# Kernel optimization log

Measured on AMD Instinct MI355X. Metric: run time of the kernel, lower is better.

## Reference

```python
import jax, jax.numpy as jnp
import numpy as np
from jax import lax

K = 12          # filterbank order (units per group)
G = 2           # number of groups / filterbanks
T_SAMP = 1.0    # samp_interval
B, S = 2048, 2048


def setup_inputs() -> dict:
    key = jax.random.key(0)
    k1, k2 = jax.random.split(key)
    x = jax.random.normal(k1, (B, S, G), dtype=jnp.float32)
    # relax in (0.2, 0.8) so sqrt(relax) and sqrt(1-relax) are well-behaved
    relax = 0.2 + 0.6 * jax.random.uniform(k2, (G,), dtype=jnp.float32)
    return {"x": x, "relax": relax}


def reference(x, relax):
    """Laguerre FilterbankCell unrolled over time with lax.scan.

    x:     [B, S, G] input sequence (one channel per filterbank group)
    relax: [G]       per-group relaxation parameter in (0,1)
    returns [B, S, G, K] filterbank outputs per timestep.
    """
    sa = jnp.sqrt(relax)            # sqrt(relax_i),    [G]
    sb = jnp.sqrt(1.0 - relax)      # sqrt(1-relax_i),  [G]

    def step(prev, xt):
        # prev: [B, G, K] previous filterbank state; xt: [B, G]
        y0 = sa[None, :] * prev[:, :, 0] + T_SAMP * sb[None, :] * xt  # [B, G]
        ys = [y0]
        for j in range(1, K):  # K is small and fixed -> unrolled lag chain
            yj = sa[None, :] * prev[:, :, j] + sa[None, :] * ys[-1] - prev[:, :, j - 1]
            ys.append(yj)
        y = jnp.stack(ys, axis=2)  # [B, G, K]
        return y, y

    init = jnp.zeros((x.shape[0], G, K), dtype=x.dtype)
    xs = jnp.moveaxis(x, 1, 0)                 # [S, B, G]
    _, outs = lax.scan(step, init, xs)         # [S, B, G, K]
    return jnp.moveaxis(outs, 0, 1)            # [B, S, G, K]
```

## Files before the change

kernel.cpp:

```cpp
#include <hip/hip_runtime.h>


#define KF 12
#define GF 2
#define BF 2048
#define SF 2048
#define CHUNKS 32
#define LCH 64
#define BG (BF * GF)

__global__ void setup_mpow(const float* __restrict__ relax, float* __restrict__ Mp) {
    const int g = blockIdx.x;
    const int t = threadIdx.x;
    __shared__ float A[KF][KF];
    const float rx = relax[g];
    const float sa = sqrtf(rx);

    if (t < KF * KF) {
        const int j = t / KF, m = t % KF;
        float v = 0.0f;
        if (m == j) {
            v = sa;
        } else if (m < j) {
            float p = 1.0f;
            for (int i = 0; i < j - m - 1; ++i) p *= sa;
            v = -(1.0f - rx) * p;
        }
        A[j][m] = v;
    }
    __syncthreads();

    for (int it = 0; it < 6; ++it) {
        float s = 0.0f;
        if (t < KF * KF) {
            const int j = t / KF, m = t % KF;
            #pragma unroll
            for (int i = 0; i < KF; ++i) s += A[j][i] * A[i][m];
        }
        __syncthreads();
        if (t < KF * KF) A[t / KF][t % KF] = s;
        __syncthreads();
    }

    if (t < KF * KF) Mp[g * KF * KF + t] = A[t / KF][t % KF];
}

__device__ __forceinline__ void fb_step(float* y, float xt, float sa, float tsb) {
    float pm1 = y[0];
    y[0] = sa * y[0] + tsb * xt;
    #pragma unroll
    for (int j = 1; j < KF; ++j) {
        const float tmp = y[j];
        y[j] = sa * tmp + sa * y[j - 1] - pm1;
        pm1 = tmp;
    }
}

__global__ void pass1_chunk_states(const float* __restrict__ x,
                                   const float* __restrict__ relax,
                                   float* __restrict__ F) {
    const int tid = blockIdx.x * blockDim.x + threadIdx.x;
    const int g = tid & 1;
    const int b = (tid >> 1) & (BF - 1);
    const int c = tid >> 12;

    const float rx = relax[g];
    const float sa = sqrtf(rx);
    const float tsb = sqrtf(1.0f - rx);

    float y[KF];
    #pragma unroll
    for (int k = 0; k < KF; ++k) y[k] = 0.0f;

    const float* xp = x + ((size_t)b * SF + (size_t)c * LCH) * GF + g;
    for (int t = 0; t < LCH; ++t) {
        fb_step(y, xp[(size_t)t * GF], sa, tsb);
    }

    float4* Fp = (float4*)(F + (((size_t)c * BF + b) * GF + g) * KF);
    Fp[0] = make_float4(y[0], y[1], y[2],  y[3]);
    Fp[1] = make_float4(y[4], y[5], y[6],  y[7]);
    Fp[2] = make_float4(y[8], y[9], y[10], y[11]);
}

__global__ void pass2_combine(float* __restrict__ F, const float* __restrict__ Mp) {
    const int tid = blockIdx.x * blockDim.x + threadIdx.x;
    const int sub = tid & 15;
    const int bg  = tid >> 4;
    const int g   = bg & 1;
    const int lane = threadIdx.x & 63;
    const int grpbase = lane & ~15;

    const int k = (sub < KF) ? sub : 0;
    float Mrow[KF];
    const float* mr = Mp + ((size_t)g * KF + k) * KF;
    #pragma unroll
    for (int m = 0; m < KF; ++m) Mrow[m] = mr[m];

    float r = 0.0f;
    for (int c = 1; c < CHUNKS; ++c) {
        float* slot = F + ((size_t)(c - 1) * BG + bg) * KF + k;
        const float f = *slot;
        float acc = f;
        #pragma unroll
        for (int m = 0; m < KF; ++m) {
            acc += Mrow[m] * __shfl(r, grpbase + m, 64);
        }
        if (sub < KF) *slot = acc;
        r = acc;
    }
}

__global__ void pass3_outputs(const float* __restrict__ x,
                              const float* __restrict__ relax,
                              const float* __restrict__ F,
                              float* __restrict__ out) {
    const int tid = blockIdx.x * blockDim.x + threadIdx.x;
    const int g = tid & 1;
    const int b = (tid >> 1) & (BF - 1);
    const int c = tid >> 12;

    const float rx = relax[g];
    const float sa = sqrtf(rx);
    const float tsb = sqrtf(1.0f - rx);

    float y[KF];
    if (c == 0) {
        #pragma unroll
        for (int k = 0; k < KF; ++k) y[k] = 0.0f;
    } else {
        const float4* Fp = (const float4*)(F + ((size_t)(c - 1) * BG + (b * GF + g)) * KF);
        const float4 a0 = Fp[0], a1 = Fp[1], a2 = Fp[2];
        y[0] = a0.x; y[1] = a0.y; y[2]  = a0.z; y[3]  = a0.w;
        y[4] = a1.x; y[5] = a1.y; y[6]  = a1.z; y[7]  = a1.w;
        y[8] = a2.x; y[9] = a2.y; y[10] = a2.z; y[11] = a2.w;
    }

    const float* xp = x + ((size_t)b * SF + (size_t)c * LCH) * GF + g;
    float* op = out + (((size_t)b * SF + (size_t)c * LCH) * GF + g) * KF;

    for (int t = 0; t < LCH; ++t) {
        fb_step(y, xp[(size_t)t * GF], sa, tsb);
        float4* o4 = (float4*)(op + (size_t)t * (GF * KF));
        o4[0] = make_float4(y[0], y[1], y[2],  y[3]);
        o4[1] = make_float4(y[4], y[5], y[6],  y[7]);
        o4[2] = make_float4(y[8], y[9], y[10], y[11]);
    }
}

extern "C" void kernel_launch(void* const* d_in, const int* in_sizes, int n_in,
                              void* d_out, int out_size, void* d_ws, size_t ws_size,
                              hipStream_t stream) {
    const float* x     = (const float*)d_in[0];
    const float* relax = (const float*)d_in[1];
    float* out = (float*)d_out;

    float* Mp = (float*)d_ws;
    float* F  = (float*)((char*)d_ws + 4096);

    setup_mpow<<<GF, 192, 0, stream>>>(relax, Mp);

    const int threads13 = BG * CHUNKS;
    pass1_chunk_states<<<threads13 / 256, 256, 0, stream>>>(x, relax, F);

    pass2_combine<<<(BG * 16) / 256, 256, 0, stream>>>(F, Mp);

    pass3_outputs<<<threads13 / 256, 256, 0, stream>>>(x, relax, F, out);
}
```

Before: 573.6 us.

## Process both groups per thread and raise chunk count for more parallelism

Each thread in pass1 and pass3 now runs the filter for both groups together, reading x as float4 and writing the 24 outputs of a timestep together. The chunk index becomes the fastest-varying thread index, and the chunk count rises to 128 (or 64 if workspace is small), with shorter chunks and a matching matrix power. This aims at more instruction-level parallelism and better load vectorization. The cost is more register pressure, a longer serial pass2 combine chain, and more scattered output stores across adjacent threads.

```diff
diff --git a/kernel.cpp b/kernel.cpp
--- a/kernel.cpp
+++ b/kernel.cpp
@@ -5,11 +5,27 @@
 #define GF 2
 #define BF 2048
 #define SF 2048
-#define CHUNKS 32
-#define LCH 64
 #define BG (BF * GF)
 
+__device__ __forceinline__ void fb_step2(float* __restrict__ y0, float* __restrict__ y1,
+                                         float x0, float x1,
+                                         float sa0, float tsb0, float sa1, float tsb1) {
+    float pm0 = y0[0], pm1 = y1[0];
+    y0[0] = fmaf(sa0, y0[0], tsb0 * x0);
+    y1[0] = fmaf(sa1, y1[0], tsb1 * x1);
+    #pragma unroll
+    for (int j = 1; j < KF; ++j) {
+        const float t0 = y0[j], t1 = y1[j];
+        y0[j] = fmaf(sa0, t0, fmaf(sa0, y0[j - 1], -pm0));
+        y1[j] = fmaf(sa1, t1, fmaf(sa1, y1[j - 1], -pm1));
+        pm0 = t0; pm1 = t1;
+    }
+}
+
+template <int NC>
 __global__ void setup_mpow(const float* __restrict__ relax, float* __restrict__ Mp) {
+    constexpr int LCH = SF / NC;
+    constexpr int LOG2L = (LCH == 16) ? 4 : ((LCH == 32) ? 5 : 6);
     const int g = blockIdx.x;
     const int t = threadIdx.x;
     __shared__ float A[KF][KF];
@@ -30,7 +46,7 @@
     }
     __syncthreads();
 
-    for (int it = 0; it < 6; ++it) {
+    for (int it = 0; it < LOG2L; ++it) {
         float s = 0.0f;
         if (t < KF * KF) {
             const int j = t / KF, m = t % KF;
@@ -45,44 +61,41 @@
     if (t < KF * KF) Mp[g * KF * KF + t] = A[t / KF][t % KF];
 }
 
-__device__ __forceinline__ void fb_step(float* y, float xt, float sa, float tsb) {
-    float pm1 = y[0];
-    y[0] = sa * y[0] + tsb * xt;
+template <int NC>
+__global__ __launch_bounds__(256, 4) void pass1_chunk_states(
+        const float* __restrict__ x, const float* __restrict__ relax,
+        float* __restrict__ F) {
+    constexpr int LCH = SF / NC;
+    const int tid = blockIdx.x * 256 + threadIdx.x;
+    const int c = tid & (NC - 1);
+    const int b = tid / NC;
+
+    const float r0 = relax[0], r1 = relax[1];
+    const float sa0 = sqrtf(r0), tsb0 = sqrtf(1.0f - r0);
+    const float sa1 = sqrtf(r1), tsb1 = sqrtf(1.0f - r1);
+
+    float y0[KF], y1[KF];
     #pragma unroll
-    for (int j = 1; j < KF; ++j) {
-        const float tmp = y[j];
-        y[j] = sa * tmp + sa * y[j - 1] - pm1;
-        pm1 = tmp;
-    }
-}
-
-__global__ void pass1_chunk_states(const float* __restrict__ x,
-                                   const float* __restrict__ relax,
-                                   float* __restrict__ F) {
-    const int tid = blockIdx.x * blockDim.x + threadIdx.x;
-    const int g = tid & 1;
-    const int b = (tid >> 1) & (BF - 1);
-    const int c = tid >> 12;
-
-    const float rx = relax[g];
-    const float sa = sqrtf(rx);
-    const float tsb = sqrtf(1.0f - rx);
-
-    float y[KF];
-    #pragma unroll
-    for (int k = 0; k < KF; ++k) y[k] = 0.0f;
-
-    const float* xp = x + ((size_t)b * SF + (size_t)c * LCH) * GF + g;
-    for (int t = 0; t < LCH; ++t) {
-        fb_step(y, xp[(size_t)t * GF], sa, tsb);
-    }
-
-    float4* Fp = (float4*)(F + (((size_t)c * BF + b) * GF + g) * KF);
-    Fp[0] = make_float4(y[0], y[1], y[2],  y[3]);
-    Fp[1] = make_float4(y[4], y[5], y[6],  y[7]);
-    Fp[2] = make_float4(y[8], y[9], y[10], y[11]);
-}
-
+    for (int k = 0; k < KF; ++k) { y0[k] = 0.0f; y1[k] = 0.0f; }
+
+    const float4* xp = (const float4*)(x + ((size_t)b * SF + (size_t)c * LCH) * GF);
+    #pragma unroll 2
+    for (int t2 = 0; t2 < LCH / 2; ++t2) {
+        const float4 xv = xp[t2];
+        fb_step2(y0, y1, xv.x, xv.y, sa0, tsb0, sa1, tsb1);
+        fb_step2(y0, y1, xv.z, xv.w, sa0, tsb0, sa1, tsb1);
+    }
+
+    float4* Fp = (float4*)(F + ((size_t)c * BF + b) * (GF * KF));
+    Fp[0] = make_float4(y0[0], y0[1], y0[2],  y0[3]);
+    Fp[1] = make_float4(y0[4], y0[5], y0[6],  y0[7]);
+    Fp[2] = make_float4(y0[8], y0[9], y0[10], y0[11]);
+    Fp[3] = make_float4(y1[0], y1[1], y1[2],  y1[3]);
+    Fp[4] = make_float4(y1[4], y1[5], y1[6],  y1[7]);
+    Fp[5] = make_float4(y1[8], y1[9], y1[10], y1[11]);
+}
+
+template <int NC>
 __global__ void pass2_combine(float* __restrict__ F, const float* __restrict__ Mp) {
     const int tid = blockIdx.x * blockDim.x + threadIdx.x;
     const int sub = tid & 15;
@@ -98,10 +111,9 @@
     for (int m = 0; m < KF; ++m) Mrow[m] = mr[m];
 
     float r = 0.0f;
-    for (int c = 1; c < CHUNKS; ++c) {
+    for (int c = 1; c < NC; ++c) {
         float* slot = F + ((size_t)(c - 1) * BG + bg) * KF + k;
-        const float f = *slot;
-        float acc = f;
+        float acc = *slot;
         #pragma unroll
         for (int m = 0; m < KF; ++m) {
             acc += Mrow[m] * __shfl(r, grpbase + m, 64);
@@ -111,41 +123,70 @@
     }
 }
 
-__global__ void pass3_outputs(const float* __restrict__ x,
-                              const float* __restrict__ relax,
-                              const float* __restrict__ F,
-                              float* __restrict__ out) {
-    const int tid = blockIdx.x * blockDim.x + threadIdx.x;
-    const int g = tid & 1;
-    const int b = (tid >> 1) & (BF - 1);
-    const int c = tid >> 12;
-
-    const float rx = relax[g];
-    const float sa = sqrtf(rx);
-    const float tsb = sqrtf(1.0f - rx);
-
-    float y[KF];
+template <int NC>
+__global__ __launch_bounds__(256, 4) void pass3_outputs(
+        const float* __restrict__ x, const float* __restrict__ relax,
+        const float* __restrict__ F, float* __restrict__ out) {
+    constexpr int LCH = SF / NC;
+    const int tid = blockIdx.x * 256 + threadIdx.x;
+    const int c = tid & (NC - 1);
+    const int b = tid / NC;
+
+    const float r0 = relax[0], r1 = relax[1];
+    const float sa0 = sqrtf(r0), tsb0 = sqrtf(1.0f - r0);
+    const float sa1 = sqrtf(r1), tsb1 = sqrtf(1.0f - r1);
+
+    float y0[KF], y1[KF];
     if (c == 0) {
         #pragma unroll
-        for (int k = 0; k < KF; ++k) y[k] = 0.0f;
+        for (int k = 0; k < KF; ++k) { y0[k] = 0.0f; y1[k] = 0.0f; }
     } else {
-        const float4* Fp = (const float4*)(F + ((size_t)(c - 1) * BG + (b * GF + g)) * KF);
+        const float4* Fp = (const float4*)(F + ((size_t)(c - 1) * BF + b) * (GF * KF));
         const float4 a0 = Fp[0], a1 = Fp[1], a2 = Fp[2];
-        y[0] = a0.x; y[1] = a0.y; y[2]  = a0.z; y[3]  = a0.w;
-        y[4] = a1.x; y[5] = a1.y; y[6]  = a1.z; y[7]  = a1.w;
-        y[8] = a2.x; y[9] = a2.y; y[10] = a2.z; y[11] = a2.w;
-    }
-
-    const float* xp = x + ((size_t)b * SF + (size_t)c * LCH) * GF + g;
-    float* op = out + (((size_t)b * SF + (size_t)c * LCH) * GF + g) * KF;
-
-    for (int t = 0; t < LCH; ++t) {
-        fb_step(y, xp[(size_t)t * GF], sa, tsb);
-        float4* o4 = (float4*)(op + (size_t)t * (GF * KF));
-        o4[0] = make_float4(y[0], y[1], y[2],  y[3]);
-        o4[1] = make_float4(y[4], y[5], y[6],  y[7]);
-        o4[2] = make_float4(y[8], y[9], y[10], y[11]);
-    }
+        const float4 a3 = Fp[3], a4 = Fp[4], a5 = Fp[5];
+        y0[0] = a0.x; y0[1] = a0.y; y0[2]  = a0.z; y0[3]  = a0.w;
+        y0[4] = a1.x; y0[5] = a1.y; y0[6]  = a1.z; y0[7]  = a1.w;
+        y0[8] = a2.x; y0[9] = a2.y; y0[10] = a2.z; y0[11] = a2.w;
+        y1[0] = a3.x; y1[1] = a3.y; y1[2]  = a3.z; y1[3]  = a3.w;
+        y1[4] = a4.x; y1[5] = a4.y; y1[6]  = a4.z; y1[7]  = a4.w;
+        y1[8] = a5.x; y1[9] = a5.y; y1[10] = a5.z; y1[11] = a5.w;
+    }
+
+    const float4* xp = (const float4*)(x + ((size_t)b * SF + (size_t)c * LCH) * GF);
+    float* op = out + ((size_t)b * SF + (size_t)c * LCH) * (GF * KF);
+
+    #pragma unroll 2
+    for (int t2 = 0; t2 < LCH / 2; ++t2) {
+        const float4 xv = xp[t2];
+
+        fb_step2(y0, y1, xv.x, xv.y, sa0, tsb0, sa1, tsb1);
+        float4* o4 = (float4*)(op + (size_t)(2 * t2) * (GF * KF));
+        o4[0] = make_float4(y0[0], y0[1], y0[2],  y0[3]);
+        o4[1] = make_float4(y0[4], y0[5], y0[6],  y0[7]);
+        o4[2] = make_float4(y0[8], y0[9], y0[10], y0[11]);
+        o4[3] = make_float4(y1[0], y1[1], y1[2],  y1[3]);
+        o4[4] = make_float4(y1[4], y1[5], y1[6],  y1[7]);
+        o4[5] = make_float4(y1[8], y1[9], y1[10], y1[11]);
+
+        fb_step2(y0, y1, xv.z, xv.w, sa0, tsb0, sa1, tsb1);
+        float4* o4b = (float4*)(op + (size_t)(2 * t2 + 1) * (GF * KF));
+        o4b[0] = make_float4(y0[0], y0[1], y0[2],  y0[3]);
+        o4b[1] = make_float4(y0[4], y0[5], y0[6],  y0[7]);
+        o4b[2] = make_float4(y0[8], y0[9], y0[10], y0[11]);
+        o4b[3] = make_float4(y1[0], y1[1], y1[2],  y1[3]);
+        o4b[4] = make_float4(y1[4], y1[5], y1[6],  y1[7]);
+        o4b[5] = make_float4(y1[8], y1[9], y1[10], y1[11]);
+    }
+}
+
+template <int NC>
+static void run_all(const float* x, const float* relax, float* out,
+                    float* Mp, float* F, hipStream_t stream) {
+    setup_mpow<NC><<<GF, 192, 0, stream>>>(relax, Mp);
+    const int threads13 = BF * NC;
+    pass1_chunk_states<NC><<<threads13 / 256, 256, 0, stream>>>(x, relax, F);
+    pass2_combine<NC><<<(BG * 16) / 256, 256, 0, stream>>>(F, Mp);
+    pass3_outputs<NC><<<threads13 / 256, 256, 0, stream>>>(x, relax, F, out);
 }
 
 extern "C" void kernel_launch(void* const* d_in, const int* in_sizes, int n_in,
@@ -158,12 +199,10 @@
     float* Mp = (float*)d_ws;
     float* F  = (float*)((char*)d_ws + 4096);
 
-    setup_mpow<<<GF, 192, 0, stream>>>(relax, Mp);
-
-    const int threads13 = BG * CHUNKS;
-    pass1_chunk_states<<<threads13 / 256, 256, 0, stream>>>(x, relax, F);
-
-    pass2_combine<<<(BG * 16) / 256, 256, 0, stream>>>(F, Mp);
-
-    pass3_outputs<<<threads13 / 256, 256, 0, stream>>>(x, relax, F, out);
-}
+    const size_t need128 = 4096 + (size_t)128 * BF * (GF * KF) * sizeof(float);
+    if (ws_size >= need128) {
+        run_all<128>(x, relax, out, Mp, F, stream);
+    } else {
+        run_all<64>(x, relax, out, Mp, F, stream);
+    }
+}
```

New measurement: 628.9 us. +9.6%, slower.
